# Kernel optimization log

Measured on AMD Instinct MI355X. Metric: run time of the kernel, lower is better.

## Reference

```python
import jax, jax.numpy as jnp
import numpy as np

B, N, E, H = 8, 1024, 768, 12
HD = E // H

def setup_inputs() -> dict:
    key = jax.random.key(0)
    k1, k2, k3, k4, k5 = jax.random.split(key, 5)
    s = 0.02
    return {
        'query': jax.random.normal(k1, (B, N, E), dtype=jnp.float32),
        'qkv_w': jax.random.normal(k2, (3 * E, E), dtype=jnp.float32) * s,
        'qkv_b': jax.random.normal(k3, (3 * E,), dtype=jnp.float32) * s,
        'out_w': jax.random.normal(k4, (E, E), dtype=jnp.float32) * s,
        'out_b': jax.random.normal(k5, (E,), dtype=jnp.float32) * s,
    }

def reference(query, qkv_w, qkv_b, out_w, out_b):
    b, n, e = query.shape
    scale = HD ** -0.5
    # torch Linear: x @ W^T + b
    qkv = query @ qkv_w.T + qkv_b              # [B,N,3E]
    qkv = qkv.reshape(b, n, 3, H, HD)
    q = qkv[:, :, 0].transpose(0, 2, 1, 3)     # [B,H,N,hd]
    k = qkv[:, :, 1].transpose(0, 2, 1, 3)
    v = qkv[:, :, 2].transpose(0, 2, 1, 3)
    attn = jnp.einsum('bhqd,bhkd->bhqk', q, k) * scale
    attn = jax.nn.softmax(attn, axis=-1)
    x = jnp.einsum('bhqk,bhkd->bhqd', attn, v)  # [B,H,N,hd]
    x = x.transpose(0, 2, 1, 3).reshape(b, n, e)
    return x @ out_w.T + out_b
```

## Files before the change

kernel.cpp:

```cpp
#include <hip/hip_runtime.h>
#include <cstdint>
#include <cstddef>

#define QSCALE 0.18033688011112042f

typedef __bf16 bf16x8 __attribute__((ext_vector_type(8)));
typedef __bf16 bf16x4 __attribute__((ext_vector_type(4)));
typedef short short4v __attribute__((ext_vector_type(4)));
typedef float floatx4 __attribute__((ext_vector_type(4)));

static __device__ __forceinline__ uint16_t f2bf(float f) {
    uint32_t u = __builtin_bit_cast(uint32_t, f);
    u += 0x7FFFu + ((u >> 16) & 1u);
    return (uint16_t)(u >> 16);
}

static __device__ __forceinline__ void st_bf16(uint16_t* p, float f) {
    *(__bf16*)p = (__bf16)f;
}

static __device__ __forceinline__ bf16x8 ld_frag(const uint16_t* p) {
    uint4 u = *(const uint4*)p;
    return __builtin_bit_cast(bf16x8, u);
}

static __device__ __forceinline__ void async_lds16(const uint16_t* g, uint16_t* l) {
    __builtin_amdgcn_global_load_lds(
        (const __attribute__((address_space(1))) void*)g,
        (__attribute__((address_space(3))) void*)l,
        16, 0, 0);
}

static __device__ __forceinline__ size_t qk_swz(int bh, int idx, int hd) {
    return (size_t)bh * 65536 + (size_t)(idx >> 4) * 1024 + (size_t)(hd >> 5) * 512
         + (size_t)((hd & 31) >> 3) * 128 + (size_t)(idx & 15) * 8 + (hd & 7);
}
static __device__ __forceinline__ size_t v_swz(int bh, int hd, int key) {
    return (size_t)bh * 65536 + (size_t)(key >> 6) * 4096 + (size_t)(hd >> 4) * 1024
         + (size_t)((key >> 4) & 3) * 256 + (size_t)((key >> 2) & 3) * 64
         + (size_t)(hd & 15) * 4 + (key & 3);
}

__global__ __launch_bounds__(256) void cast3_kernel(
    const float* __restrict__ a, uint16_t* __restrict__ da, int na8,
    const float* __restrict__ b, uint16_t* __restrict__ db, int nb8,
    const float* __restrict__ c, uint16_t* __restrict__ dc, int nc8)
{
    int i = blockIdx.x * 256 + threadIdx.x;
    const float* src; uint16_t* dst; int idx;
    if (i < na8)                { src = a; dst = da; idx = i; }
    else if (i < na8 + nb8)     { src = b; dst = db; idx = i - na8; }
    else if (i < na8 + nb8 + nc8){ src = c; dst = dc; idx = i - na8 - nb8; }
    else return;
    const float4* p = (const float4*)src + (size_t)2 * idx;
    float4 x = p[0], y = p[1];
    uint32_t w0 = (uint32_t)f2bf(x.x) | ((uint32_t)f2bf(x.y) << 16);
    uint32_t w1 = (uint32_t)f2bf(x.z) | ((uint32_t)f2bf(x.w) << 16);
    uint32_t w2 = (uint32_t)f2bf(y.x) | ((uint32_t)f2bf(y.y) << 16);
    uint32_t w3 = (uint32_t)f2bf(y.z) | ((uint32_t)f2bf(y.w) << 16);
    uint4 v; v.x = w0; v.y = w1; v.z = w2; v.w = w3;
    *((uint4*)dst + idx) = v;
}

__global__ __launch_bounds__(256) void gemm_qkv_kernel(
    const uint16_t* __restrict__ X,
    const uint16_t* __restrict__ W,
    const float* __restrict__ bias,
    uint16_t* __restrict__ Qs, uint16_t* __restrict__ Ks, uint16_t* __restrict__ Vs)
{
    __shared__ __align__(16) uint16_t As[128 * 32];
    __shared__ __align__(16) uint16_t Bs[128 * 32];
    const int tid = threadIdx.x;
    const int wave = tid >> 6, lane = tid & 63;
    const int L = lane & 15, quad = lane >> 4;
    const int wM = (wave >> 1) * 64, wN = (wave & 1) * 64;
    const int bm = blockIdx.x * 128;
    const int bn = blockIdx.y * 128;

    floatx4 zero4 = {0.f, 0.f, 0.f, 0.f};
    floatx4 acc[4][4];
    #pragma unroll
    for (int i = 0; i < 4; ++i)
        #pragma unroll
        for (int j = 0; j < 4; ++j) acc[i][j] = zero4;

    const int srow = tid >> 2;
    const int scol = (tid & 3) * 8;
    const uint16_t* xp0 = X + (size_t)(bm + srow) * 768 + scol;
    const uint16_t* xp1 = xp0 + (size_t)64 * 768;
    const uint16_t* wp0 = W + (size_t)(bn + srow) * 768 + scol;
    const uint16_t* wp1 = wp0 + (size_t)64 * 768;
    uint16_t* lA0 = As + wave * 512;
    uint16_t* lA1 = As + 2048 + wave * 512;
    uint16_t* lB0 = Bs + wave * 512;
    uint16_t* lB1 = Bs + 2048 + wave * 512;

    for (int k0 = 0; k0 < 768; k0 += 32) {
        __syncthreads();
        async_lds16(xp0 + k0, lA0);
        async_lds16(xp1 + k0, lA1);
        async_lds16(wp0 + k0, lB0);
        async_lds16(wp1 + k0, lB1);
        __syncthreads();
        bf16x8 af[4], bfr[4];
        #pragma unroll
        for (int mi = 0; mi < 4; ++mi) af[mi]  = ld_frag(&As[(wM + mi * 16 + L) * 32 + quad * 8]);
        #pragma unroll
        for (int ni = 0; ni < 4; ++ni) bfr[ni] = ld_frag(&Bs[(wN + ni * 16 + L) * 32 + quad * 8]);
        #pragma unroll
        for (int mi = 0; mi < 4; ++mi)
            #pragma unroll
            for (int ni = 0; ni < 4; ++ni)
                acc[mi][ni] = __builtin_amdgcn_mfma_f32_16x16x32_bf16(
                    af[mi], bfr[ni], acc[mi][ni], 0, 0, 0);
    }

    const int part = bn / 768;
    #pragma unroll
    for (int ni = 0; ni < 4; ++ni) {
        int col = bn + wN + ni * 16 + L;
        int c = col - part * 768;
        int h = c >> 6, hd = c & 63;
        float bv = bias[col];
        #pragma unroll
        for (int mi = 0; mi < 4; ++mi) {
            #pragma unroll
            for (int r = 0; r < 4; ++r) {
                int m = bm + wM + mi * 16 + quad * 4 + r;
                int b = m >> 10, ns = m & 1023;
                int bh = b * 12 + h;
                float v = acc[mi][ni][r] + bv;
                if (part == 0)      st_bf16(&Qs[qk_swz(bh, ns, hd)], v * QSCALE);
                else if (part == 1) st_bf16(&Ks[qk_swz(bh, ns, hd)], v);
                else                st_bf16(&Vs[v_swz(bh, hd, ns)], v);
            }
        }
    }
}

__global__ __launch_bounds__(256) void attn_kernel(
    const uint16_t* __restrict__ Qs,
    const uint16_t* __restrict__ Ks,
    const uint16_t* __restrict__ Vs,
    uint16_t* __restrict__ Ob)
{
    const int tid = threadIdx.x;
    const int wave = tid >> 6, lane = tid & 63;
    const int L = lane & 15, quad = lane >> 4;
    const int bh = blockIdx.x;
    const int qt = blockIdx.y;
    const int b = bh / 12, h = bh - b * 12;
    const int q0 = qt * 128 + wave * 32;

    floatx4 zero4 = {0.f, 0.f, 0.f, 0.f};

    const uint16_t* qbase = Qs + (size_t)bh * 65536 + (size_t)lane * 8;
    bf16x8 aq[2][2];
    #pragma unroll
    for (int st = 0; st < 2; ++st) {
        const uint16_t* qp = qbase + (size_t)(qt * 8 + wave * 2 + st) * 1024;
        aq[st][0] = ld_frag(qp);
        aq[st][1] = ld_frag(qp + 512);
    }

    floatx4 accO[2][4];
    #pragma unroll
    for (int st = 0; st < 2; ++st)
        #pragma unroll
        for (int t = 0; t < 4; ++t) accO[st][t] = zero4;
    float lacc[2] = {0.f, 0.f};

    const uint16_t* kbase = Ks + (size_t)bh * 65536 + (size_t)lane * 8;
    const uint16_t* vbase = Vs + (size_t)bh * 65536 + (size_t)lane * 4;

    for (int j = 0; j < 16; ++j) {
        bf16x8 ka[4][2];
        #pragma unroll
        for (int kc = 0; kc < 4; ++kc) {
            const uint16_t* kp = kbase + (size_t)(j * 4 + kc) * 1024;
            ka[kc][0] = ld_frag(kp);
            ka[kc][1] = ld_frag(kp + 512);
        }
        short4v va[4][4];
        const uint16_t* vp = vbase + (size_t)j * 4096;
        #pragma unroll
        for (int t = 0; t < 4; ++t)
            #pragma unroll
            for (int kc = 0; kc < 4; ++kc)
                va[kc][t] = *(const short4v*)(vp + t * 1024 + kc * 256);

        floatx4 c[2][4];
        #pragma unroll
        for (int st = 0; st < 2; ++st)
            #pragma unroll
            for (int kc = 0; kc < 4; ++kc) {
                floatx4 z = zero4;
                z = __builtin_amdgcn_mfma_f32_16x16x32_bf16(ka[kc][0], aq[st][0], z, 0, 0, 0);
                z = __builtin_amdgcn_mfma_f32_16x16x32_bf16(ka[kc][1], aq[st][1], z, 0, 0, 0);
                c[st][kc] = z;
            }

        short4v pb[2][4];
        #pragma unroll
        for (int st = 0; st < 2; ++st)
            #pragma unroll
            for (int kc = 0; kc < 4; ++kc) {
                float p0 = __builtin_amdgcn_exp2f(c[st][kc][0]);
                float p1 = __builtin_amdgcn_exp2f(c[st][kc][1]);
                float p2 = __builtin_amdgcn_exp2f(c[st][kc][2]);
                float p3 = __builtin_amdgcn_exp2f(c[st][kc][3]);
                lacc[st] += (p0 + p1) + (p2 + p3);
                bf16x4 t4;
                t4.x = (__bf16)p0; t4.y = (__bf16)p1;
                t4.z = (__bf16)p2; t4.w = (__bf16)p3;
                pb[st][kc] = __builtin_bit_cast(short4v, t4);
            }

        #pragma unroll
        for (int st = 0; st < 2; ++st)
            #pragma unroll
            for (int t = 0; t < 4; ++t)
                #pragma unroll
                for (int kc = 0; kc < 4; ++kc)
                    accO[st][t] = __builtin_amdgcn_mfma_f32_16x16x16bf16_1k(
                        va[kc][t], pb[st][kc], accO[st][t], 0, 0, 0);
    }

    #pragma unroll
    for (int st = 0; st < 2; ++st) {
        float sum = lacc[st];
        sum += __shfl_xor(sum, 16);
        sum += __shfl_xor(sum, 32);
        float inv = 1.f / sum;
        uint16_t* orow = Ob + ((size_t)b * 1024 + q0 + st * 16 + L) * 768 + h * 64 + quad * 4;
        #pragma unroll
        for (int t = 0; t < 4; ++t) {
            bf16x4 o4;
            o4.x = (__bf16)(accO[st][t][0] * inv);
            o4.y = (__bf16)(accO[st][t][1] * inv);
            o4.z = (__bf16)(accO[st][t][2] * inv);
            o4.w = (__bf16)(accO[st][t][3] * inv);
            *(uint2*)(orow + t * 16) = __builtin_bit_cast(uint2, o4);
        }
    }
}

__global__ __launch_bounds__(256) void gemm_out_kernel(
    const uint16_t* __restrict__ X,
    const uint16_t* __restrict__ W,
    const float* __restrict__ bias,
    float* __restrict__ out)
{
    __shared__ __align__(16) uint16_t As[128 * 32];
    __shared__ __align__(16) uint16_t Bs[128 * 32];
    const int tid = threadIdx.x;
    const int wave = tid >> 6, lane = tid & 63;
    const int L = lane & 15, quad = lane >> 4;
    const int wM = (wave >> 1) * 64, wN = (wave & 1) * 64;
    const int bm = blockIdx.x * 128;
    const int bn = blockIdx.y * 128;

    floatx4 zero4 = {0.f, 0.f, 0.f, 0.f};
    floatx4 acc[4][4];
    #pragma unroll
    for (int i = 0; i < 4; ++i)
        #pragma unroll
        for (int j = 0; j < 4; ++j) acc[i][j] = zero4;

    const int srow = tid >> 2;
    const int scol = (tid & 3) * 8;
    const uint16_t* xp0 = X + (size_t)(bm + srow) * 768 + scol;
    const uint16_t* xp1 = xp0 + (size_t)64 * 768;
    const uint16_t* wp0 = W + (size_t)(bn + srow) * 768 + scol;
    const uint16_t* wp1 = wp0 + (size_t)64 * 768;
    uint16_t* lA0 = As + wave * 512;
    uint16_t* lA1 = As + 2048 + wave * 512;
    uint16_t* lB0 = Bs + wave * 512;
    uint16_t* lB1 = Bs + 2048 + wave * 512;

    for (int k0 = 0; k0 < 768; k0 += 32) {
        __syncthreads();
        async_lds16(xp0 + k0, lA0);
        async_lds16(xp1 + k0, lA1);
        async_lds16(wp0 + k0, lB0);
        async_lds16(wp1 + k0, lB1);
        __syncthreads();
        bf16x8 af[4], bfr[4];
        #pragma unroll
        for (int mi = 0; mi < 4; ++mi) af[mi]  = ld_frag(&As[(wM + mi * 16 + L) * 32 + quad * 8]);
        #pragma unroll
        for (int ni = 0; ni < 4; ++ni) bfr[ni] = ld_frag(&Bs[(wN + ni * 16 + L) * 32 + quad * 8]);
        #pragma unroll
        for (int mi = 0; mi < 4; ++mi)
            #pragma unroll
            for (int ni = 0; ni < 4; ++ni)
                acc[mi][ni] = __builtin_amdgcn_mfma_f32_16x16x32_bf16(
                    af[mi], bfr[ni], acc[mi][ni], 0, 0, 0);
    }

    #pragma unroll
    for (int ni = 0; ni < 4; ++ni) {
        int col = bn + wN + ni * 16 + L;
        float bv = bias[col];
        #pragma unroll
        for (int mi = 0; mi < 4; ++mi)
            #pragma unroll
            for (int r = 0; r < 4; ++r) {
                int m = bm + wM + mi * 16 + quad * 4 + r;
                out[(size_t)m * 768 + col] = acc[mi][ni][r] + bv;
            }
    }
}

extern "C" void kernel_launch(void* const* d_in, const int* in_sizes, int n_in,
                              void* d_out, int out_size, void* d_ws, size_t ws_size,
                              hipStream_t stream) {
    const float* query = (const float*)d_in[0];
    const float* qkv_w = (const float*)d_in[1];
    const float* qkv_b = (const float*)d_in[2];
    const float* out_w = (const float*)d_in[3];
    const float* out_b = (const float*)d_in[4];
    float* out = (float*)d_out;

    uint8_t* ws = (uint8_t*)d_ws;
    uint16_t* Xb  = (uint16_t*)(ws);
    uint16_t* W1b = (uint16_t*)(ws + 12582912);
    uint16_t* W2b = (uint16_t*)(ws + 16121856);
    uint16_t* Qsw = (uint16_t*)(ws + 17301504);
    uint16_t* Ksw = (uint16_t*)(ws + 29884416);
    uint16_t* Vsw = (uint16_t*)(ws + 42467328);
    uint16_t* Ab  = Xb;

    cast3_kernel<<<4224, 256, 0, stream>>>(query, Xb, 786432,
                                           qkv_w, W1b, 221184,
                                           out_w, W2b, 73728);
    gemm_qkv_kernel<<<dim3(64, 18), 256, 0, stream>>>(Xb, W1b, qkv_b, Qsw, Ksw, Vsw);
    attn_kernel<<<dim3(96, 8), 256, 0, stream>>>(Qsw, Ksw, Vsw, Ab);
    gemm_out_kernel<<<dim3(64, 6), 256, 0, stream>>>(Ab, W2b, out_b, out);
}
```

Before: 196.0 us.

## Store GEMM operands in MFMA fragment order and load directly to registers

```diff
diff --git a/kernel.cpp b/kernel.cpp
--- a/kernel.cpp
+++ b/kernel.cpp
@@ -24,16 +24,9 @@
     return __builtin_bit_cast(bf16x8, u);
 }
 
-static __device__ __forceinline__ void async_lds16(const uint16_t* g, uint16_t* l) {
-    __builtin_amdgcn_global_load_lds(
-        (const __attribute__((address_space(1))) void*)g,
-        (__attribute__((address_space(3))) void*)l,
-        16, 0, 0);
-}
-
-static __device__ __forceinline__ size_t qk_swz(int bh, int idx, int hd) {
-    return (size_t)bh * 65536 + (size_t)(idx >> 4) * 1024 + (size_t)(hd >> 5) * 512
-         + (size_t)((hd & 31) >> 3) * 128 + (size_t)(idx & 15) * 8 + (hd & 7);
+static __device__ __forceinline__ size_t frag_off(int row, int k, int K16) {
+    return (size_t)(row >> 4) * K16 + (size_t)(k >> 5) * 512
+         + (size_t)((k >> 3) & 3) * 128 + (size_t)(row & 15) * 8 + (k & 7);
 }
 static __device__ __forceinline__ size_t v_swz(int bh, int hd, int key) {
     return (size_t)bh * 65536 + (size_t)(key >> 6) * 4096 + (size_t)(hd >> 4) * 1024
@@ -52,24 +45,24 @@
     else if (i < na8 + nb8)     { src = b; dst = db; idx = i - na8; }
     else if (i < na8 + nb8 + nc8){ src = c; dst = dc; idx = i - na8 - nb8; }
     else return;
-    const float4* p = (const float4*)src + (size_t)2 * idx;
+    int row = idx / 96;
+    int k = (idx - row * 96) * 8;
+    const float4* p = (const float4*)(src + (size_t)row * 768 + k);
     float4 x = p[0], y = p[1];
     uint32_t w0 = (uint32_t)f2bf(x.x) | ((uint32_t)f2bf(x.y) << 16);
     uint32_t w1 = (uint32_t)f2bf(x.z) | ((uint32_t)f2bf(x.w) << 16);
     uint32_t w2 = (uint32_t)f2bf(y.x) | ((uint32_t)f2bf(y.y) << 16);
     uint32_t w3 = (uint32_t)f2bf(y.z) | ((uint32_t)f2bf(y.w) << 16);
     uint4 v; v.x = w0; v.y = w1; v.z = w2; v.w = w3;
-    *((uint4*)dst + idx) = v;
+    *(uint4*)(dst + frag_off(row, k, 12288)) = v;
 }
 
 __global__ __launch_bounds__(256) void gemm_qkv_kernel(
-    const uint16_t* __restrict__ X,
-    const uint16_t* __restrict__ W,
+    const uint16_t* __restrict__ Xf,
+    const uint16_t* __restrict__ Wf,
     const float* __restrict__ bias,
     uint16_t* __restrict__ Qs, uint16_t* __restrict__ Ks, uint16_t* __restrict__ Vs)
 {
-    __shared__ __align__(16) uint16_t As[128 * 32];
-    __shared__ __align__(16) uint16_t Bs[128 * 32];
     const int tid = threadIdx.x;
     const int wave = tid >> 6, lane = tid & 63;
     const int L = lane & 15, quad = lane >> 4;
@@ -77,6 +70,15 @@
     const int bm = blockIdx.x * 128;
     const int bn = blockIdx.y * 128;
 
+    const uint16_t* ap[4];
+    const uint16_t* bp[4];
+    #pragma unroll
+    for (int mi = 0; mi < 4; ++mi)
+        ap[mi] = Xf + (size_t)(bm + wM + mi * 16) * 768 + lane * 8;
+    #pragma unroll
+    for (int ni = 0; ni < 4; ++ni)
+        bp[ni] = Wf + (size_t)(bn + wN + ni * 16) * 768 + lane * 8;
+
     floatx4 zero4 = {0.f, 0.f, 0.f, 0.f};
     floatx4 acc[4][4];
     #pragma unroll
@@ -84,36 +86,50 @@
         #pragma unroll
         for (int j = 0; j < 4; ++j) acc[i][j] = zero4;
 
-    const int srow = tid >> 2;
-    const int scol = (tid & 3) * 8;
-    const uint16_t* xp0 = X + (size_t)(bm + srow) * 768 + scol;
-    const uint16_t* xp1 = xp0 + (size_t)64 * 768;
-    const uint16_t* wp0 = W + (size_t)(bn + srow) * 768 + scol;
-    const uint16_t* wp1 = wp0 + (size_t)64 * 768;
-    uint16_t* lA0 = As + wave * 512;
-    uint16_t* lA1 = As + 2048 + wave * 512;
-    uint16_t* lB0 = Bs + wave * 512;
-    uint16_t* lB1 = Bs + 2048 + wave * 512;
-
-    for (int k0 = 0; k0 < 768; k0 += 32) {
-        __syncthreads();
-        async_lds16(xp0 + k0, lA0);
-        async_lds16(xp1 + k0, lA1);
-        async_lds16(wp0 + k0, lB0);
-        async_lds16(wp1 + k0, lB1);
-        __syncthreads();
-        bf16x8 af[4], bfr[4];
-        #pragma unroll
-        for (int mi = 0; mi < 4; ++mi) af[mi]  = ld_frag(&As[(wM + mi * 16 + L) * 32 + quad * 8]);
-        #pragma unroll
-        for (int ni = 0; ni < 4; ++ni) bfr[ni] = ld_frag(&Bs[(wN + ni * 16 + L) * 32 + quad * 8]);
+    bf16x8 a0[4], b0[4], a1[4], b1[4];
+    #pragma unroll
+    for (int mi = 0; mi < 4; ++mi) a0[mi] = ld_frag(ap[mi]);
+    #pragma unroll
+    for (int ni = 0; ni < 4; ++ni) b0[ni] = ld_frag(bp[ni]);
+
+    for (int it = 0; it < 11; ++it) {
+        #pragma unroll
+        for (int mi = 0; mi < 4; ++mi) a1[mi] = ld_frag(ap[mi] + 512);
+        #pragma unroll
+        for (int ni = 0; ni < 4; ++ni) b1[ni] = ld_frag(bp[ni] + 512);
         #pragma unroll
         for (int mi = 0; mi < 4; ++mi)
             #pragma unroll
             for (int ni = 0; ni < 4; ++ni)
-                acc[mi][ni] = __builtin_amdgcn_mfma_f32_16x16x32_bf16(
-                    af[mi], bfr[ni], acc[mi][ni], 0, 0, 0);
-    }
+                acc[mi][ni] = __builtin_amdgcn_mfma_f32_16x16x32_bf16(a0[mi], b0[ni], acc[mi][ni], 0, 0, 0);
+        #pragma unroll
+        for (int mi = 0; mi < 4; ++mi) a0[mi] = ld_frag(ap[mi] + 1024);
+        #pragma unroll
+        for (int ni = 0; ni < 4; ++ni) b0[ni] = ld_frag(bp[ni] + 1024);
+        #pragma unroll
+        for (int mi = 0; mi < 4; ++mi)
+            #pragma unroll
+            for (int ni = 0; ni < 4; ++ni)
+                acc[mi][ni] = __builtin_amdgcn_mfma_f32_16x16x32_bf16(a1[mi], b1[ni], acc[mi][ni], 0, 0, 0);
+        #pragma unroll
+        for (int mi = 0; mi < 4; ++mi) ap[mi] += 1024;
+        #pragma unroll
+        for (int ni = 0; ni < 4; ++ni) bp[ni] += 1024;
+    }
+    #pragma unroll
+    for (int mi = 0; mi < 4; ++mi) a1[mi] = ld_frag(ap[mi] + 512);
+    #pragma unroll
+    for (int ni = 0; ni < 4; ++ni) b1[ni] = ld_frag(bp[ni] + 512);
+    #pragma unroll
+    for (int mi = 0; mi < 4; ++mi)
+        #pragma unroll
+        for (int ni = 0; ni < 4; ++ni)
+            acc[mi][ni] = __builtin_amdgcn_mfma_f32_16x16x32_bf16(a0[mi], b0[ni], acc[mi][ni], 0, 0, 0);
+    #pragma unroll
+    for (int mi = 0; mi < 4; ++mi)
+        #pragma unroll
+        for (int ni = 0; ni < 4; ++ni)
+            acc[mi][ni] = __builtin_amdgcn_mfma_f32_16x16x32_bf16(a1[mi], b1[ni], acc[mi][ni], 0, 0, 0);
 
     const int part = bn / 768;
     #pragma unroll
@@ -130,8 +146,8 @@
                 int b = m >> 10, ns = m & 1023;
                 int bh = b * 12 + h;
                 float v = acc[mi][ni][r] + bv;
-                if (part == 0)      st_bf16(&Qs[qk_swz(bh, ns, hd)], v * QSCALE);
-                else if (part == 1) st_bf16(&Ks[qk_swz(bh, ns, hd)], v);
+                if (part == 0)      st_bf16(&Qs[(size_t)bh * 65536 + frag_off(ns, hd, 1024)], v * QSCALE);
+                else if (part == 1) st_bf16(&Ks[(size_t)bh * 65536 + frag_off(ns, hd, 1024)], v);
                 else                st_bf16(&Vs[v_swz(bh, hd, ns)], v);
             }
         }
@@ -142,7 +158,7 @@
     const uint16_t* __restrict__ Qs,
     const uint16_t* __restrict__ Ks,
     const uint16_t* __restrict__ Vs,
-    uint16_t* __restrict__ Ob)
+    uint16_t* __restrict__ Of)
 {
     const int tid = threadIdx.x;
     const int wave = tid >> 6, lane = tid & 63;
@@ -150,7 +166,6 @@
     const int bh = blockIdx.x;
     const int qt = blockIdx.y;
     const int b = bh / 12, h = bh - b * 12;
-    const int q0 = qt * 128 + wave * 32;
 
     floatx4 zero4 = {0.f, 0.f, 0.f, 0.f};
 
@@ -232,7 +247,8 @@
         sum += __shfl_xor(sum, 16);
         sum += __shfl_xor(sum, 32);
         float inv = 1.f / sum;
-        uint16_t* orow = Ob + ((size_t)b * 1024 + q0 + st * 16 + L) * 768 + h * 64 + quad * 4;
+        size_t obase = (size_t)(b * 64 + qt * 8 + wave * 2 + st) * 12288
+                     + (size_t)L * 8 + (quad & 1) * 4;
         #pragma unroll
         for (int t = 0; t < 4; ++t) {
             bf16x4 o4;
@@ -240,73 +256,94 @@
             o4.y = (__bf16)(accO[st][t][1] * inv);
             o4.z = (__bf16)(accO[st][t][2] * inv);
             o4.w = (__bf16)(accO[st][t][3] * inv);
-            *(uint2*)(orow + t * 16) = __builtin_bit_cast(uint2, o4);
+            *(uint2*)(Of + obase + (size_t)(h * 2 + (t >> 1)) * 512
+                      + (size_t)((t * 2 + (quad >> 1)) & 3) * 128) = __builtin_bit_cast(uint2, o4);
         }
     }
 }
 
 __global__ __launch_bounds__(256) void gemm_out_kernel(
-    const uint16_t* __restrict__ X,
-    const uint16_t* __restrict__ W,
+    const uint16_t* __restrict__ Xf,
+    const uint16_t* __restrict__ Wf,
     const float* __restrict__ bias,
     float* __restrict__ out)
 {
-    __shared__ __align__(16) uint16_t As[128 * 32];
-    __shared__ __align__(16) uint16_t Bs[128 * 32];
     const int tid = threadIdx.x;
     const int wave = tid >> 6, lane = tid & 63;
     const int L = lane & 15, quad = lane >> 4;
-    const int wM = (wave >> 1) * 64, wN = (wave & 1) * 64;
     const int bm = blockIdx.x * 128;
-    const int bn = blockIdx.y * 128;
+    const int bn = blockIdx.y * 64;
+
+    const uint16_t* ap[2];
+    const uint16_t* bp[4];
+    #pragma unroll
+    for (int mi = 0; mi < 2; ++mi)
+        ap[mi] = Xf + (size_t)(bm + wave * 32 + mi * 16) * 768 + lane * 8;
+    #pragma unroll
+    for (int ni = 0; ni < 4; ++ni)
+        bp[ni] = Wf + (size_t)(bn + ni * 16) * 768 + lane * 8;
 
     floatx4 zero4 = {0.f, 0.f, 0.f, 0.f};
-    floatx4 acc[4][4];
-    #pragma unroll
-    for (int i = 0; i < 4; ++i)
+    floatx4 acc[2][4];
+    #pragma unroll
+    for (int i = 0; i < 2; ++i)
         #pragma unroll
         for (int j = 0; j < 4; ++j) acc[i][j] = zero4;
 
-    const int srow = tid >> 2;
-    const int scol = (tid & 3) * 8;
-    const uint16_t* xp0 = X + (size_t)(bm + srow) * 768 + scol;
-    const uint16_t* xp1 = xp0 + (size_t)64 * 768;
-    const uint16_t* wp0 = W + (size_t)(bn + srow) * 768 + scol;
-    const uint16_t* wp1 = wp0 + (size_t)64 * 768;
-    uint16_t* lA0 = As + wave * 512;
-    uint16_t* lA1 = As + 2048 + wave * 512;
-    uint16_t* lB0 = Bs + wave * 512;
-    uint16_t* lB1 = Bs + 2048 + wave * 512;
-
-    for (int k0 = 0; k0 < 768; k0 += 32) {
-        __syncthreads();
-        async_lds16(xp0 + k0, lA0);
-        async_lds16(xp1 + k0, lA1);
-        async_lds16(wp0 + k0, lB0);
-        async_lds16(wp1 + k0, lB1);
-        __syncthreads();
-        bf16x8 af[4], bfr[4];
-        #pragma unroll
-        for (int mi = 0; mi < 4; ++mi) af[mi]  = ld_frag(&As[(wM + mi * 16 + L) * 32 + quad * 8]);
-        #pragma unroll
-        for (int ni = 0; ni < 4; ++ni) bfr[ni] = ld_frag(&Bs[(wN + ni * 16 + L) * 32 + quad * 8]);
-        #pragma unroll
-        for (int mi = 0; mi < 4; ++mi)
+    bf16x8 a0[2], b0[4], a1[2], b1[4];
+    #pragma unroll
+    for (int mi = 0; mi < 2; ++mi) a0[mi] = ld_frag(ap[mi]);
+    #pragma unroll
+    for (int ni = 0; ni < 4; ++ni) b0[ni] = ld_frag(bp[ni]);
+
+    for (int it = 0; it < 11; ++it) {
+        #pragma unroll
+        for (int mi = 0; mi < 2; ++mi) a1[mi] = ld_frag(ap[mi] + 512);
+        #pragma unroll
+        for (int ni = 0; ni < 4; ++ni) b1[ni] = ld_frag(bp[ni] + 512);
+        #pragma unroll
+        for (int mi = 0; mi < 2; ++mi)
             #pragma unroll
             for (int ni = 0; ni < 4; ++ni)
-                acc[mi][ni] = __builtin_amdgcn_mfma_f32_16x16x32_bf16(
-                    af[mi], bfr[ni], acc[mi][ni], 0, 0, 0);
-    }
+                acc[mi][ni] = __builtin_amdgcn_mfma_f32_16x16x32_bf16(a0[mi], b0[ni], acc[mi][ni], 0, 0, 0);
+        #pragma unroll
+        for (int mi = 0; mi < 2; ++mi) a0[mi] = ld_frag(ap[mi] + 1024);
+        #pragma unroll
+        for (int ni = 0; ni < 4; ++ni) b0[ni] = ld_frag(bp[ni] + 1024);
+        #pragma unroll
+        for (int mi = 0; mi < 2; ++mi)
+            #pragma unroll
+            for (int ni = 0; ni < 4; ++ni)
+                acc[mi][ni] = __builtin_amdgcn_mfma_f32_16x16x32_bf16(a1[mi], b1[ni], acc[mi][ni], 0, 0, 0);
+        #pragma unroll
+        for (int mi = 0; mi < 2; ++mi) ap[mi] += 1024;
+        #pragma unroll
+        for (int ni = 0; ni < 4; ++ni) bp[ni] += 1024;
+    }
+    #pragma unroll
+    for (int mi = 0; mi < 2; ++mi) a1[mi] = ld_frag(ap[mi] + 512);
+    #pragma unroll
+    for (int ni = 0; ni < 4; ++ni) b1[ni] = ld_frag(bp[ni] + 512);
+    #pragma unroll
+    for (int mi = 0; mi < 2; ++mi)
+        #pragma unroll
+        for (int ni = 0; ni < 4; ++ni)
+            acc[mi][ni] = __builtin_amdgcn_mfma_f32_16x16x32_bf16(a0[mi], b0[ni], acc[mi][ni], 0, 0, 0);
+    #pragma unroll
+    for (int mi = 0; mi < 2; ++mi)
+        #pragma unroll
+        for (int ni = 0; ni < 4; ++ni)
+            acc[mi][ni] = __builtin_amdgcn_mfma_f32_16x16x32_bf16(a1[mi], b1[ni], acc[mi][ni], 0, 0, 0);
 
     #pragma unroll
     for (int ni = 0; ni < 4; ++ni) {
-        int col = bn + wN + ni * 16 + L;
+        int col = bn + ni * 16 + L;
         float bv = bias[col];
         #pragma unroll
-        for (int mi = 0; mi < 4; ++mi)
+        for (int mi = 0; mi < 2; ++mi)
             #pragma unroll
             for (int r = 0; r < 4; ++r) {
-                int m = bm + wM + mi * 16 + quad * 4 + r;
+                int m = bm + wave * 32 + mi * 16 + quad * 4 + r;
                 out[(size_t)m * 768 + col] = acc[mi][ni][r] + bv;
             }
     }
@@ -323,18 +360,18 @@
     float* out = (float*)d_out;
 
     uint8_t* ws = (uint8_t*)d_ws;
-    uint16_t* Xb  = (uint16_t*)(ws);
-    uint16_t* W1b = (uint16_t*)(ws + 12582912);
-    uint16_t* W2b = (uint16_t*)(ws + 16121856);
+    uint16_t* Xf  = (uint16_t*)(ws);
+    uint16_t* W1f = (uint16_t*)(ws + 12582912);
+    uint16_t* W2f = (uint16_t*)(ws + 16121856);
     uint16_t* Qsw = (uint16_t*)(ws + 17301504);
     uint16_t* Ksw = (uint16_t*)(ws + 29884416);
     uint16_t* Vsw = (uint16_t*)(ws + 42467328);
-    uint16_t* Ab  = Xb;
-
-    cast3_kernel<<<4224, 256, 0, stream>>>(query, Xb, 786432,
-                                           qkv_w, W1b, 221184,
-                                           out_w, W2b, 73728);
-    gemm_qkv_kernel<<<dim3(64, 18), 256, 0, stream>>>(Xb, W1b, qkv_b, Qsw, Ksw, Vsw);
-    attn_kernel<<<dim3(96, 8), 256, 0, stream>>>(Qsw, Ksw, Vsw, Ab);
-    gemm_out_kernel<<<dim3(64, 6), 256, 0, stream>>>(Ab, W2b, out_b, out);
-}
+    uint16_t* Of  = Xf;
+
+    cast3_kernel<<<4224, 256, 0, stream>>>(query, Xf, 786432,
+                                           qkv_w, W1f, 221184,
+                                           out_w, W2f, 73728);
+    gemm_qkv_kernel<<<dim3(64, 18), 256, 0, stream>>>(Xf, W1f, qkv_b, Qsw, Ksw, Vsw);
+    attn_kernel<<<dim3(96, 8), 256, 0, stream>>>(Qsw, Ksw, Vsw, Of);
+    gemm_out_kernel<<<dim3(64, 12), 256, 0, stream>>>(Of, W2f, out_b, out);
+}
```

After: 216.7 us. 1.11x slower.
